# Optimization experiments

Measured on AMD Instinct MI355X. Metric: run time of the kernel, lower is better.

Reference implementation:

```python
import jax, jax.numpy as jnp
import numpy as np

DIM = 1024
Q_HEADS = 16
KV_HEADS = 4
DIM_HEAD = DIM // Q_HEADS  # 64
SOFTCLAMP = 50.0
EPS = 1e-8


def rotate_half(x):
    x_even = x[..., ::2]
    x_odd = x[..., 1::2]
    return jnp.stack([-x_odd, x_even], axis=-1).reshape(x.shape)


def setup_inputs() -> dict:
    key = jax.random.key(0)
    ks = jax.random.split(key, 10)
    B, S = 1, 2048
    dim_q = DIM_HEAD * Q_HEADS   # 1024
    dim_kv = DIM_HEAD * KV_HEADS  # 256
    std = 0.02
    x = jax.random.normal(ks[0], (B, S, DIM), dtype=jnp.float32)
    positions = jnp.broadcast_to(jnp.arange(S, dtype=jnp.int32)[None, :], (B, S))
    # causal mask: True = disallowed (torch semantics: allowed = ~attn_mask)
    attn_mask = jnp.triu(jnp.ones((S, S), dtype=bool), k=1)
    return {
        "x": x,
        "positions": positions,
        "attn_mask": attn_mask,
        "Wq": jax.random.normal(ks[1], (DIM, dim_q), jnp.float32) * std,
        "Wk": jax.random.normal(ks[2], (DIM, dim_kv), jnp.float32) * std,
        "Wv": jax.random.normal(ks[3], (DIM, dim_kv), jnp.float32) * std,
        "Wo": jax.random.normal(ks[4], (dim_q, DIM), jnp.float32) * std,
        "Wg": jax.random.normal(ks[5], (DIM, Q_HEADS), jnp.float32) * std,
        "Wm": jax.random.normal(ks[6], (DIM, KV_HEADS), jnp.float32) * std,
        "bm": jnp.zeros((KV_HEADS,), jnp.float32),
        "Wvr": jax.random.normal(ks[7], (DIM, dim_kv), jnp.float32) * std,
        "k_scale": jnp.ones((KV_HEADS, DIM_HEAD), jnp.float32),
    }


def reference(x, positions, attn_mask, Wq, Wk, Wv, Wo, Wg, Wm, bm, Wvr, k_scale):
    b, s, _ = x.shape
    h, qh, dh = KV_HEADS, Q_HEADS, DIM_HEAD
    g = qh // h

    q = (x @ Wq).reshape(b, s, qh, dh).transpose(0, 2, 1, 3)  # [b,qh,s,dh]
    k = (x @ Wk).reshape(b, s, h, dh).transpose(0, 2, 1, 3)   # [b,h,s,dh]
    v = (x @ Wv).reshape(b, s, h, dh).transpose(0, 2, 1, 3)

    # value-residual gating: v = lerp(v, residual_v, mix)
    residual_v = (x @ Wvr).reshape(b, s, h, dh).transpose(0, 2, 1, 3)
    mix = jax.nn.sigmoid(x @ Wm + bm).transpose(0, 2, 1)[..., None]  # [b,h,s,1]
    v = v + mix * (residual_v - v)

    # multi-head RMSNorm on k
    rms = jnp.sqrt(jnp.mean(k * k, axis=-1, keepdims=True) + EPS)
    k = k / rms * k_scale[None, :, None, :]

    # rotary embeddings (identical for all heads -> broadcast over head dim)
    inv_freq = 1.0 / (10000.0 ** (jnp.arange(0, dh, 2, dtype=jnp.float32) / dh))
    freqs = positions.astype(jnp.float32)[..., None] * inv_freq  # [b,s,dh/2]
    cos = jnp.repeat(jnp.cos(freqs), 2, axis=-1)[:, None, :, :]  # [b,1,s,dh]
    sin = jnp.repeat(jnp.sin(freqs), 2, axis=-1)[:, None, :, :]
    q = q * cos + rotate_half(q) * sin
    k = k * cos + rotate_half(k) * sin

    # grouped-query attention with softclamped scores
    scale = dh ** -0.5
    qg = q.reshape(b, h, g, s, dh)
    sim = jnp.einsum('bhgqd,bhkd->bhgqk', qg, k) * scale
    sim = jnp.tanh(sim / SOFTCLAMP) * SOFTCLAMP
    allowed = ~attn_mask  # [s,s]
    sim = jnp.where(allowed[None, None, None, :, :], sim, jnp.finfo(sim.dtype).min)
    attn = jax.nn.softmax(sim, axis=-1)
    out = jnp.einsum('bhgqk,bhkd->bhgqd', attn, v).reshape(b, qh, s, dh)

    # per-query-head sigmoid gates
    gates = jax.nn.sigmoid(x @ Wg).transpose(0, 2, 1)[..., None]  # [b,qh,s,1]
    out = out * gates

    out = out.transpose(0, 2, 1, 3).reshape(b, s, qh * dh)
    return out @ Wo
```

## Files before the change

kernel.cpp:

```cpp
#include <hip/hip_runtime.h>
#include <hip/hip_bf16.h>
#include <math.h>

typedef unsigned short u16;
typedef unsigned int u32;
typedef __attribute__((ext_vector_type(8))) __bf16 bf16x8;
typedef __attribute__((ext_vector_type(4))) float f32x4;

__device__ inline u16 f2bf(float f) {
  u32 b = __float_as_uint(f);
  b += 0x7FFFu + ((b >> 16) & 1u);
  return (u16)(b >> 16);
}
__device__ inline float bf2f(u16 b) { return __uint_as_float((u32)b << 16); }

__global__ __launch_bounds__(256) void cvt_bf16_k(
    const float* __restrict__ in, u16* __restrict__ out) {
  int i = (blockIdx.x * 256 + threadIdx.x) * 8;
  float4 v0 = *(const float4*)&in[i];
  float4 v1 = *(const float4*)&in[i + 4];
  uint4 pk;
  pk.x = (u32)f2bf(v0.x) | ((u32)f2bf(v0.y) << 16);
  pk.y = (u32)f2bf(v0.z) | ((u32)f2bf(v0.w) << 16);
  pk.z = (u32)f2bf(v1.x) | ((u32)f2bf(v1.y) << 16);
  pk.w = (u32)f2bf(v1.z) | ((u32)f2bf(v1.w) << 16);
  *(uint4*)&out[i] = pk;
}

__global__ __launch_bounds__(256) void prep_w_k(
    const float* __restrict__ Wq, const float* __restrict__ Wk,
    const float* __restrict__ Wv, const float* __restrict__ Wvr,
    const float* __restrict__ Wo, const float* __restrict__ Wg,
    const float* __restrict__ Wm, u16* __restrict__ WallT,
    u16* __restrict__ WoT) {
  __shared__ float tile[32][33];
  int k0 = blockIdx.x * 32;
  int ybl = blockIdx.y;
  int tx = threadIdx.x, ty = threadIdx.y;
  const float* src;
  int scol, sN, drow;
  u16* dst;
  if (ybl >= 60) {
    src = Wo; scol = (ybl - 60) * 32; sN = 1024; dst = WoT; drow = scol;
  } else {
    int n0 = ybl * 32;
    if (n0 >= 1792) {
#pragma unroll
      for (int j = 0; j < 4; ++j) {
        int n = n0 + ty * 4 + j, j2 = n - 1792, k = k0 + tx;
        float val = (j2 < 16) ? Wg[(size_t)k * 16 + j2]
                  : (j2 < 20) ? Wm[(size_t)k * 4 + (j2 - 16)] : 0.f;
        WallT[(size_t)n * 1024 + k] = f2bf(val);
      }
      return;
    }
    dst = WallT; drow = n0;
    if (n0 < 1024) { src = Wq; scol = n0; sN = 1024; }
    else if (n0 < 1280) { src = Wk; scol = n0 - 1024; sN = 256; }
    else if (n0 < 1536) { src = Wv; scol = n0 - 1280; sN = 256; }
    else { src = Wvr; scol = n0 - 1536; sN = 256; }
  }
#pragma unroll
  for (int j = 0; j < 4; ++j)
    tile[ty * 4 + j][tx] = src[(size_t)(k0 + ty * 4 + j) * sN + scol + tx];
  __syncthreads();
#pragma unroll
  for (int j = 0; j < 4; ++j)
    dst[(size_t)(drow + ty * 4 + j) * 1024 + k0 + tx] = f2bf(tile[tx][ty * 4 + j]);
}

__global__ __launch_bounds__(256) void rope_tab_k(
    const int* __restrict__ positions, float* __restrict__ tab) {
  int idx = blockIdx.x * 256 + threadIdx.x;
  int s = idx >> 5, f = idx & 31;
  float inv = __expf(-(float)f * (9.210340371976184f / 32.f));
  float ang = (float)positions[s] * inv;
  tab[(size_t)s * 64 + f] = cosf(ang);
  tab[(size_t)s * 64 + 32 + f] = sinf(ang);
}

template <int BM, bool BF16_OUT>
__global__ __launch_bounds__(512) void gemm_bf16_k(
    const u16* __restrict__ A, const u16* __restrict__ Bt, void* __restrict__ Cv,
    int M, int N, int K) {
  constexpr int MI = BM / 32;
  __shared__ __align__(16) u16 As[BM * 64];
  __shared__ __align__(16) u16 Bs[128 * 64];
  int tid = threadIdx.x;
  int w = tid >> 6, l = tid & 63;
  int wr = w >> 2, wc = w & 3;
  int lr = l & 15, lg = l >> 4;
  int m0 = blockIdx.y * BM, n0 = blockIdx.x * 128;
  f32x4 zero = {0.f, 0.f, 0.f, 0.f};
  f32x4 acc[MI][2];
#pragma unroll
  for (int mi = 0; mi < MI; ++mi)
#pragma unroll
    for (int ni = 0; ni < 2; ++ni) acc[mi][ni] = zero;

  for (int kt = 0; kt < K; kt += 64) {
    __syncthreads();
#pragma unroll
    for (int c = 0; c < BM * 64 / (8 * 512); ++c) {
      int idx = c * 512 + tid;
      int row = idx >> 3, k0 = (idx & 7) * 8;
      *(uint4*)&As[row * 64 + k0] =
          *(const uint4*)&A[(size_t)(m0 + row) * K + kt + k0];
    }
#pragma unroll
    for (int c = 0; c < 2; ++c) {
      int idx = c * 512 + tid;
      int row = idx >> 3, k0 = (idx & 7) * 8;
      *(uint4*)&Bs[row * 64 + k0] =
          *(const uint4*)&Bt[(size_t)(n0 + row) * K + kt + k0];
    }
    __syncthreads();
#pragma unroll
    for (int kw = 0; kw < 2; ++kw) {
      bf16x8 af[MI], bfr[2];
#pragma unroll
      for (int mi = 0; mi < MI; ++mi)
        af[mi] = *(const bf16x8*)&As[(wr * (BM / 2) + mi * 16 + lr) * 64 + kw * 32 + lg * 8];
#pragma unroll
      for (int ni = 0; ni < 2; ++ni)
        bfr[ni] = *(const bf16x8*)&Bs[(wc * 32 + ni * 16 + lr) * 64 + kw * 32 + lg * 8];
#pragma unroll
      for (int mi = 0; mi < MI; ++mi)
#pragma unroll
        for (int ni = 0; ni < 2; ++ni)
          acc[mi][ni] = __builtin_amdgcn_mfma_f32_16x16x32_bf16(
              af[mi], bfr[ni], acc[mi][ni], 0, 0, 0);
    }
  }
#pragma unroll
  for (int mi = 0; mi < MI; ++mi)
#pragma unroll
    for (int ni = 0; ni < 2; ++ni)
#pragma unroll
      for (int r = 0; r < 4; ++r) {
        int row = m0 + wr * (BM / 2) + mi * 16 + lg * 4 + r;
        int col = n0 + wc * 32 + ni * 16 + lr;
        if (BF16_OUT)
          ((u16*)Cv)[(size_t)row * N + col] = f2bf(acc[mi][ni][r]);
        else
          ((float*)Cv)[(size_t)row * N + col] = acc[mi][ni][r];
      }
}

__global__ __launch_bounds__(256) void postproc_k(
    const float* __restrict__ bm, const float* __restrict__ ksc,
    const float* __restrict__ rtab, u16* __restrict__ qkvrb,
    u16* __restrict__ kb, u16* __restrict__ vb, float* __restrict__ g_out) {
  int s = blockIdx.x, tid = threadIdx.x;
  int lane = tid & 63, w = tid >> 6;
  u16* row = qkvrb + (size_t)s * 1920;
  const float* tr = rtab + (size_t)s * 64;
  if (tid < 16)
    g_out[s * 16 + tid] = 1.f / (1.f + __expf(-bf2f(row[1792 + tid])));
  int h = w, d = lane;
  float c = tr[d >> 1], sn = tr[32 + (d >> 1)];
  {
    float mixv = 1.f / (1.f + __expf(-(bf2f(row[1808 + h]) + bm[h])));
    float vv = bf2f(row[1280 + h * 64 + d]);
    float rv = bf2f(row[1536 + h * 64 + d]);
    vb[((size_t)h * 2048 + s) * 64 + d] = f2bf(vv + mixv * (rv - vv));
  }
  {
    float kv = bf2f(row[1024 + h * 64 + d]);
    float ss = kv * kv;
#pragma unroll
    for (int off = 32; off > 0; off >>= 1) ss += __shfl_xor(ss, off);
    float rms = sqrtf(ss * (1.f / 64.f) + 1e-8f);
    float kn = kv / rms * ksc[h * 64 + d];
    float partner = __shfl_xor(kn, 1);
    kb[((size_t)h * 2048 + s) * 64 + d] =
        f2bf((d & 1) ? fmaf(kn, c, partner * sn) : fmaf(kn, c, -partner * sn));
  }
#pragma unroll
  for (int r = 0; r < 4; ++r) {
    int e = r * 256 + tid;
    int dq = e & 63;
    float cq = tr[dq >> 1], sq = tr[32 + (dq >> 1)];
    float qv = bf2f(row[e]);
    float partner = __shfl_xor(qv, 1);
    float qr = (e & 1) ? fmaf(qv, cq, partner * sq) : fmaf(qv, cq, -partner * sq);
    row[e] = f2bf(qr * 0.125f);
  }
}

#define TPAD 66
__global__ __launch_bounds__(256) void vtrans_k(const u16* __restrict__ vb,
                                               u16* __restrict__ vtb) {
  __shared__ u16 tile[64 * TPAD];
  int h = blockIdx.y, s0 = blockIdx.x * 64;
  int t = threadIdx.x;
  {
    int r = t >> 2, cb = (t & 3) * 16;
    const u16* src = vb + ((size_t)h * 2048 + s0 + r) * 64 + cb;
    *(uint4*)&tile[r * TPAD + cb] = *(const uint4*)src;
    *(uint4*)&tile[r * TPAD + cb + 8] = *(const uint4*)(src + 8);
  }
  __syncthreads();
  int d = t >> 2, sb = (t & 3) * 16;
  u16 vals[16];
#pragma unroll
  for (int j = 0; j < 16; ++j) vals[j] = tile[(sb + j) * TPAD + d];
  uint4 a, b;
  a.x = (u32)vals[0] | ((u32)vals[1] << 16);
  a.y = (u32)vals[2] | ((u32)vals[3] << 16);
  a.z = (u32)vals[4] | ((u32)vals[5] << 16);
  a.w = (u32)vals[6] | ((u32)vals[7] << 16);
  b.x = (u32)vals[8] | ((u32)vals[9] << 16);
  b.y = (u32)vals[10] | ((u32)vals[11] << 16);
  b.z = (u32)vals[12] | ((u32)vals[13] << 16);
  b.w = (u32)vals[14] | ((u32)vals[15] << 16);
  u16* dst = vtb + ((size_t)h * 64 + d) * 2048 + s0 + sb;
  *(uint4*)dst = a;
  *(uint4*)(dst + 8) = b;
}

#define KPAD 72
__global__ __launch_bounds__(512) void attn_k(
    const u16* __restrict__ qkvrb, const u16* __restrict__ kb,
    const u16* __restrict__ vtb, const float* __restrict__ g,
    u16* __restrict__ aob) {
  __shared__ __align__(16) u16 smem[18432];
  int head = blockIdx.x, hkv = head >> 2;
  int tid = threadIdx.x;
  int w = tid >> 6, l = tid & 63;
  int grp = w >> 2, wi = w & 3;
  int lr = l & 15, lg = l >> 4;
  int gtid = wi * 64 + l;
  int skey = gtid >> 2, sdb = (gtid & 3) * 16;
  u16* Ks = smem + grp * 9216;
  u16* Vt = smem + grp * 9216 + 4608;
  float* mbuf = (float*)smem;
  f32x4 zero = {0.f, 0.f, 0.f, 0.f};
  const float C1 = 0.057707801635558534f;
  const float C2 = -144.26950408889634f;
  int src_a = lr + (lg & 1) * 32, src_b = src_a + 16;
  bool hi = (lg & 2) != 0;
#pragma unroll 1
  for (int half = 0; half < 2; ++half) {
    int rb = half ? (int)blockIdx.y : (31 - (int)blockIdx.y);
    int row0 = rb * 64;
    const u16* qrow = qkvrb + (size_t)(row0 + wi * 16 + lr) * 1920 + head * 64;
    bf16x8 qf0 = *(const bf16x8*)&qrow[lg * 8];
    bf16x8 qf1 = *(const bf16x8*)&qrow[32 + lg * 8];
    f32x4 acc_o[4];
#pragma unroll
    for (int nd = 0; nd < 4; ++nd) acc_o[nd] = zero;
    float l_part = 0.f;
    int qglob = row0 + wi * 16 + lr;
    int c = grp;
    uint4 rk0, rk1, rv0, rv1;
    if (c <= rb) {
      const u16* kp = kb + ((size_t)hkv * 2048 + c * 64 + skey) * 64 + sdb;
      rk0 = *(const uint4*)kp;
      rk1 = *(const uint4*)(kp + 8);
      const u16* vp = vtb + ((size_t)(hkv * 64 + skey)) * 2048 + c * 64 + sdb;
      rv0 = *(const uint4*)vp;
      rv1 = *(const uint4*)(vp + 8);
    }
    int nmax = (rb >> 1) + 1;
#pragma unroll 1
    for (int i = 0; i < nmax; ++i, c += 2) {
      bool valid = (c <= rb);
      if (valid) {
        *(uint4*)&Ks[skey * KPAD + sdb] = rk0;
        *(uint4*)&Ks[skey * KPAD + sdb + 8] = rk1;
        *(uint4*)&Vt[skey * KPAD + sdb] = rv0;
        *(uint4*)&Vt[skey * KPAD + sdb + 8] = rv1;
      }
      __syncthreads();
      if (valid && c + 2 <= rb) {
        int nb = (c + 2) * 64;
        const u16* kp = kb + ((size_t)hkv * 2048 + nb + skey) * 64 + sdb;
        rk0 = *(const uint4*)kp;
        rk1 = *(const uint4*)(kp + 8);
        const u16* vp = vtb + ((size_t)(hkv * 64 + skey)) * 2048 + nb + sdb;
        rv0 = *(const uint4*)vp;
        rv1 = *(const uint4*)(vp + 8);
      }
      if (valid) {
        int kbase = c * 64;
        __builtin_amdgcn_s_setprio(1);
        f32x4 sa[4];
#pragma unroll
        for (int ni = 0; ni < 4; ++ni) {
          bf16x8 a0 = *(const bf16x8*)&Ks[(ni * 16 + lr) * KPAD + lg * 8];
          bf16x8 a1 = *(const bf16x8*)&Ks[(ni * 16 + lr) * KPAD + 32 + lg * 8];
          f32x4 t = __builtin_amdgcn_mfma_f32_16x16x32_bf16(a0, qf0, zero, 0, 0, 0);
          sa[ni] = __builtin_amdgcn_mfma_f32_16x16x32_bf16(a1, qf1, t, 0, 0, 0);
        }
        bool diag = (c == rb);
        u32 pkw[4][2];
#pragma unroll
        for (int ni = 0; ni < 4; ++ni) {
          float pv[4];
#pragma unroll
          for (int r = 0; r < 4; ++r) {
            float sv = sa[ni][r];
            float e = __builtin_amdgcn_exp2f(sv * C1);
            float p = __builtin_amdgcn_exp2f(C2 * __builtin_amdgcn_rcpf(e + 1.f));
            if (diag && (kbase + ni * 16 + lg * 4 + r) > qglob) p = 0.f;
            pv[r] = p;
            l_part += p;
          }
          asm("v_cvt_pk_bf16_f32 %0, %1, %2" : "=v"(pkw[ni][0]) : "v"(pv[0]), "v"(pv[1]));
          asm("v_cvt_pk_bf16_f32 %0, %1, %2" : "=v"(pkw[ni][1]) : "v"(pv[2]), "v"(pv[3]));
        }
        union { u32 w[4]; bf16x8 v; } pf0, pf1;
        {
          u32 t0[4], t1[4], t2[4], t3[4];
#define GATHER(T, NI)                          \
          T[0] = __shfl((int)pkw[NI][0], src_a);   \
          T[1] = __shfl((int)pkw[NI][1], src_a);   \
          T[2] = __shfl((int)pkw[NI][0], src_b);   \
          T[3] = __shfl((int)pkw[NI][1], src_b);
          GATHER(t0, 0)
          GATHER(t1, 1)
          GATHER(t2, 2)
          GATHER(t3, 3)
#undef GATHER
#pragma unroll
          for (int kq = 0; kq < 4; ++kq) {
            pf0.w[kq] = hi ? t1[kq] : t0[kq];
            pf1.w[kq] = hi ? t3[kq] : t2[kq];
          }
        }
#pragma unroll
        for (int nd = 0; nd < 4; ++nd) {
          bf16x8 v0 = *(const bf16x8*)&Vt[(nd * 16 + lr) * KPAD + lg * 8];
          bf16x8 v1 = *(const bf16x8*)&Vt[(nd * 16 + lr) * KPAD + 32 + lg * 8];
          acc_o[nd] = __builtin_amdgcn_mfma_f32_16x16x32_bf16(pf0.v, v0, acc_o[nd], 0, 0, 0);
          acc_o[nd] = __builtin_amdgcn_mfma_f32_16x16x32_bf16(pf1.v, v1, acc_o[nd], 0, 0, 0);
        }
        __builtin_amdgcn_s_setprio(0);
      }
      __syncthreads();
    }
    l_part += __shfl_xor(l_part, 16);
    l_part += __shfl_xor(l_part, 32);
    if (grp == 1) {
      float* mb = mbuf + (size_t)gtid * 17;
#pragma unroll
      for (int nd = 0; nd < 4; ++nd)
#pragma unroll
        for (int r = 0; r < 4; ++r) mb[nd * 4 + r] = acc_o[nd][r];
      mb[16] = l_part;
    }
    __syncthreads();
    if (grp == 0) {
      const float* mb = mbuf + (size_t)gtid * 17;
      float lt = l_part + mb[16];
#pragma unroll
      for (int r = 0; r < 4; ++r) {
        int row = row0 + wi * 16 + lg * 4 + r;
        float lv = __shfl(lt, lg * 4 + r);
        float sc = g[row * 16 + head] * __builtin_amdgcn_rcpf(lv);
#pragma unroll
        for (int nd = 0; nd < 4; ++nd)
          aob[(size_t)row * 1024 + head * 64 + nd * 16 + lr] =
              f2bf((acc_o[nd][r] + mb[nd * 4 + r]) * sc);
      }
    }
    __syncthreads();
  }
}

extern "C" void kernel_launch(void* const* d_in, const int* in_sizes, int n_in,
                              void* d_out, int out_size, void* d_ws,
                              size_t ws_size, hipStream_t stream) {
  const float* x = (const float*)d_in[0];
  const int* positions = (const int*)d_in[1];
  const float* Wq = (const float*)d_in[3];
  const float* Wk = (const float*)d_in[4];
  const float* Wv = (const float*)d_in[5];
  const float* Wo = (const float*)d_in[6];
  const float* Wg = (const float*)d_in[7];
  const float* Wm = (const float*)d_in[8];
  const float* bm = (const float*)d_in[9];
  const float* Wvr = (const float*)d_in[10];
  const float* ksc = (const float*)d_in[11];
  float* out = (float*)d_out;

  u16* xb = (u16*)d_ws;
  u16* WallT = xb + (size_t)2048 * 1024;
  u16* WoT = WallT + (size_t)1920 * 1024;
  u16* qkvrb = WoT + (size_t)1024 * 1024;
  u16* kbuf = qkvrb + (size_t)2048 * 1920;
  u16* vbuf = kbuf + (size_t)4 * 2048 * 64;
  u16* vtb = vbuf + (size_t)4 * 2048 * 64;
  float* gbuf = (float*)(vtb + (size_t)4 * 2048 * 64);
  float* rtab = gbuf + (size_t)2048 * 16;
  u16* aob = xb;

  cvt_bf16_k<<<1024, 256, 0, stream>>>(x, xb);
  prep_w_k<<<dim3(32, 92), dim3(32, 8), 0, stream>>>(Wq, Wk, Wv, Wvr, Wo, Wg,
                                                     Wm, WallT, WoT);
  rope_tab_k<<<256, 256, 0, stream>>>(positions, rtab);
  gemm_bf16_k<128, true><<<dim3(15, 16), 512, 0, stream>>>(xb, WallT, qkvrb,
                                                           2048, 1920, 1024);
  postproc_k<<<2048, 256, 0, stream>>>(bm, ksc, rtab, qkvrb, kbuf, vbuf, gbuf);
  vtrans_k<<<dim3(32, 4), 256, 0, stream>>>(vbuf, vtb);
  attn_k<<<dim3(16, 16), 512, 0, stream>>>(qkvrb, kbuf, vtb, gbuf, aob);
  gemm_bf16_k<64, false><<<dim3(8, 32), 512, 0, stream>>>(aob, WoT, out, 2048,
                                                          1024, 1024);
}
```

Measured before the change: 106.8 us.

## Merge prep kernels into one launch and double-buffer attention K/V tiles

The three prep kernels (x to bf16 conversion, weight transpose and conversion, rope table) become one kernel that picks its role from the block index, removing two launches. The attention kernel gets two LDS buffers per group for K/V tiles. The next tile is written into the alternate buffer after compute, so each iteration needs one barrier instead of two. LDS per block doubles to 72 KB, which may limit how many blocks fit per CU.

```diff
diff --git a/kernel.cpp b/kernel.cpp
--- a/kernel.cpp
+++ b/kernel.cpp
@@ -14,29 +14,40 @@
 }
 __device__ inline float bf2f(u16 b) { return __uint_as_float((u32)b << 16); }
 
-__global__ __launch_bounds__(256) void cvt_bf16_k(
-    const float* __restrict__ in, u16* __restrict__ out) {
-  int i = (blockIdx.x * 256 + threadIdx.x) * 8;
-  float4 v0 = *(const float4*)&in[i];
-  float4 v1 = *(const float4*)&in[i + 4];
-  uint4 pk;
-  pk.x = (u32)f2bf(v0.x) | ((u32)f2bf(v0.y) << 16);
-  pk.y = (u32)f2bf(v0.z) | ((u32)f2bf(v0.w) << 16);
-  pk.z = (u32)f2bf(v1.x) | ((u32)f2bf(v1.y) << 16);
-  pk.w = (u32)f2bf(v1.z) | ((u32)f2bf(v1.w) << 16);
-  *(uint4*)&out[i] = pk;
-}
-
-__global__ __launch_bounds__(256) void prep_w_k(
+__global__ __launch_bounds__(256) void prep_all_k(
+    const float* __restrict__ x, const int* __restrict__ positions,
     const float* __restrict__ Wq, const float* __restrict__ Wk,
     const float* __restrict__ Wv, const float* __restrict__ Wvr,
     const float* __restrict__ Wo, const float* __restrict__ Wg,
-    const float* __restrict__ Wm, u16* __restrict__ WallT,
-    u16* __restrict__ WoT) {
+    const float* __restrict__ Wm, u16* __restrict__ xb,
+    u16* __restrict__ WallT, u16* __restrict__ WoT, float* __restrict__ rtab) {
   __shared__ float tile[32][33];
-  int k0 = blockIdx.x * 32;
-  int ybl = blockIdx.y;
-  int tx = threadIdx.x, ty = threadIdx.y;
+  int bid = blockIdx.x, tid = threadIdx.x;
+  if (bid < 1024) {
+    int i = (bid * 256 + tid) * 8;
+    float4 v0 = *(const float4*)&x[i];
+    float4 v1 = *(const float4*)&x[i + 4];
+    uint4 pk;
+    pk.x = (u32)f2bf(v0.x) | ((u32)f2bf(v0.y) << 16);
+    pk.y = (u32)f2bf(v0.z) | ((u32)f2bf(v0.w) << 16);
+    pk.z = (u32)f2bf(v1.x) | ((u32)f2bf(v1.y) << 16);
+    pk.w = (u32)f2bf(v1.z) | ((u32)f2bf(v1.w) << 16);
+    *(uint4*)&xb[i] = pk;
+    return;
+  }
+  if (bid >= 3968) {
+    int idx = (bid - 3968) * 256 + tid;
+    int s = idx >> 5, f = idx & 31;
+    float inv = __expf(-(float)f * (9.210340371976184f / 32.f));
+    float ang = (float)positions[s] * inv;
+    rtab[(size_t)s * 64 + f] = cosf(ang);
+    rtab[(size_t)s * 64 + 32 + f] = sinf(ang);
+    return;
+  }
+  int b2 = bid - 1024;
+  int k0 = (b2 & 31) * 32;
+  int ybl = b2 >> 5;
+  int tx = tid & 31, ty = tid >> 5;
   const float* src;
   int scol, sN, drow;
   u16* dst;
@@ -67,16 +78,6 @@
 #pragma unroll
   for (int j = 0; j < 4; ++j)
     dst[(size_t)(drow + ty * 4 + j) * 1024 + k0 + tx] = f2bf(tile[tx][ty * 4 + j]);
-}
-
-__global__ __launch_bounds__(256) void rope_tab_k(
-    const int* __restrict__ positions, float* __restrict__ tab) {
-  int idx = blockIdx.x * 256 + threadIdx.x;
-  int s = idx >> 5, f = idx & 31;
-  float inv = __expf(-(float)f * (9.210340371976184f / 32.f));
-  float ang = (float)positions[s] * inv;
-  tab[(size_t)s * 64 + f] = cosf(ang);
-  tab[(size_t)s * 64 + 32 + f] = sinf(ang);
 }
 
 template <int BM, bool BF16_OUT>
@@ -224,7 +225,7 @@
     const u16* __restrict__ qkvrb, const u16* __restrict__ kb,
     const u16* __restrict__ vtb, const float* __restrict__ g,
     u16* __restrict__ aob) {
-  __shared__ __align__(16) u16 smem[18432];
+  __shared__ __align__(16) u16 smem[36864];
   int head = blockIdx.x, hkv = head >> 2;
   int tid = threadIdx.x;
   int w = tid >> 6, l = tid & 63;
@@ -232,8 +233,7 @@
   int lr = l & 15, lg = l >> 4;
   int gtid = wi * 64 + l;
   int skey = gtid >> 2, sdb = (gtid & 3) * 16;
-  u16* Ks = smem + grp * 9216;
-  u16* Vt = smem + grp * 9216 + 4608;
+  u16* KsBase = smem + grp * 18432;
   float* mbuf = (float*)smem;
   f32x4 zero = {0.f, 0.f, 0.f, 0.f};
   const float C1 = 0.057707801635558534f;
@@ -261,19 +261,18 @@
       const u16* vp = vtb + ((size_t)(hkv * 64 + skey)) * 2048 + c * 64 + sdb;
       rv0 = *(const uint4*)vp;
       rv1 = *(const uint4*)(vp + 8);
-    }
+      *(uint4*)&KsBase[skey * KPAD + sdb] = rk0;
+      *(uint4*)&KsBase[skey * KPAD + sdb + 8] = rk1;
+      *(uint4*)&KsBase[4608 + skey * KPAD + sdb] = rv0;
+      *(uint4*)&KsBase[4608 + skey * KPAD + sdb + 8] = rv1;
+    }
+    __syncthreads();
     int nmax = (rb >> 1) + 1;
 #pragma unroll 1
     for (int i = 0; i < nmax; ++i, c += 2) {
       bool valid = (c <= rb);
-      if (valid) {
-        *(uint4*)&Ks[skey * KPAD + sdb] = rk0;
-        *(uint4*)&Ks[skey * KPAD + sdb + 8] = rk1;
-        *(uint4*)&Vt[skey * KPAD + sdb] = rv0;
-        *(uint4*)&Vt[skey * KPAD + sdb + 8] = rv1;
-      }
-      __syncthreads();
-      if (valid && c + 2 <= rb) {
+      bool nvalid = (c + 2 <= rb);
+      if (nvalid) {
         int nb = (c + 2) * 64;
         const u16* kp = kb + ((size_t)hkv * 2048 + nb + skey) * 64 + sdb;
         rk0 = *(const uint4*)kp;
@@ -283,6 +282,8 @@
         rv1 = *(const uint4*)(vp + 8);
       }
       if (valid) {
+        u16* Ks = KsBase + (i & 1) * 9216;
+        u16* Vt = Ks + 4608;
         int kbase = c * 64;
         __builtin_amdgcn_s_setprio(1);
         f32x4 sa[4];
@@ -338,6 +339,13 @@
         }
         __builtin_amdgcn_s_setprio(0);
       }
+      if (nvalid) {
+        u16* Ksn = KsBase + ((i & 1) ^ 1) * 9216;
+        *(uint4*)&Ksn[skey * KPAD + sdb] = rk0;
+        *(uint4*)&Ksn[skey * KPAD + sdb + 8] = rk1;
+        *(uint4*)&Ksn[4608 + skey * KPAD + sdb] = rv0;
+        *(uint4*)&Ksn[4608 + skey * KPAD + sdb + 8] = rv1;
+      }
       __syncthreads();
     }
     l_part += __shfl_xor(l_part, 16);
@@ -396,10 +404,8 @@
   float* rtab = gbuf + (size_t)2048 * 16;
   u16* aob = xb;
 
-  cvt_bf16_k<<<1024, 256, 0, stream>>>(x, xb);
-  prep_w_k<<<dim3(32, 92), dim3(32, 8), 0, stream>>>(Wq, Wk, Wv, Wvr, Wo, Wg,
-                                                     Wm, WallT, WoT);
-  rope_tab_k<<<256, 256, 0, stream>>>(positions, rtab);
+  prep_all_k<<<4224, 256, 0, stream>>>(x, positions, Wq, Wk, Wv, Wvr, Wo, Wg,
+                                       Wm, xb, WallT, WoT, rtab);
   gemm_bf16_k<128, true><<<dim3(15, 16), 512, 0, stream>>>(xb, WallT, qkvrb,
                                                            2048, 1920, 1024);
   postproc_k<<<2048, 256, 0, stream>>>(bm, ksc, rtab, qkvrb, kbuf, vbuf, gbuf);
```

New measurement: 100.4 us. 6.0% less time.
